# Performance work log

Hardware: AMD Instinct MI355X
Metric: run time of the kernel (lower is better)

## Reference

```python
import jax, jax.numpy as jnp
import numpy as np

B, D_IN, D_OUT, N_SUBNET, G = 16384, 512, 512, 8, 2


def setup_inputs() -> dict:
    key = jax.random.key(0)
    k_x, k_g, k_w = jax.random.split(key, 3)
    x = jax.random.normal(k_x, (B, D_IN), dtype=jnp.float32)
    groups = jax.random.randint(k_g, (B, G), 0, N_SUBNET, dtype=jnp.int32)
    # per-expert Dense params (the 'subnets')
    W = jax.random.normal(k_w, (N_SUBNET, D_IN, D_OUT), dtype=jnp.float32) * (1.0 / np.sqrt(D_IN))
    b = jnp.zeros((N_SUBNET, D_OUT), dtype=jnp.float32)
    return {"x": x, "groups": groups, "W": W, "b": b}


def reference(x, groups, W, b):
    """SubnetGate: one-hot gated dispatch to per-group subnets + combine.

    Faithful math: gates = one_hot(groups[:, group_col], n_subnet);
    out = sum_e gates[:, e] * subnet_e(x). Since gates are one-hot the
    combine selects exactly one expert output per row (gate weight 1.0).
    """
    group_col = 0
    n_subnet = W.shape[0]
    idx_group = groups[:, group_col]                     # [B]
    gates = jax.nn.one_hot(idx_group, n_subnet, dtype=x.dtype)  # [B, E]
    # run every expert on the full batch (dense reference for the
    # gather-compute-scatter kernel), then gate-combine
    expert_out = jnp.einsum("bi,eio->beo", x, W) + b[None, :, :]  # [B, E, O]
    out = jnp.einsum("be,beo->bo", gates, expert_out)             # [B, O]
    return out
```

## Files before the change

### kernel.cpp

```cpp
#include <hip/hip_runtime.h>
#include <hip/hip_bf16.h>


#define NROWS   16384
#define KDIM    512
#define NDIM    512
#define NEXP    8
#define BM      256
#define BN      128
#define NT_PER  4
#define KT_PER  8
#define MC_PER  9
#define TILE_ELEMS (BN * 64)
#define WS_ROWLIST_OFF 4096
#define WS_WT_OFF      (4096 + NEXP * NROWS * 4)
#define WS_XG_OFF      (WS_WT_OFF + (size_t)NEXP * NT_PER * KT_PER * TILE_ELEMS * 2)
#define WS_NEEDED      (WS_XG_OFF + (size_t)NROWS * KDIM * 2)

typedef __bf16        bf16x8 __attribute__((ext_vector_type(8)));
typedef float         f32x4  __attribute__((ext_vector_type(4)));
typedef unsigned int  u32x4  __attribute__((ext_vector_type(4)));

__device__ __forceinline__ unsigned int f2bf_u(float f) {
    unsigned int u = __builtin_bit_cast(unsigned int, f);
    return (u + 0x7FFFu + ((u >> 16) & 1u)) >> 16;
}

__device__ __forceinline__ void gl_lds16(const void* g, void* l) {
    __builtin_amdgcn_global_load_lds(
        (const __attribute__((address_space(1))) unsigned int*)g,
        (__attribute__((address_space(3))) unsigned int*)l, 16, 0, 0);
}

__device__ __forceinline__ bf16x8 pack_bf8(f32x4 lo, f32x4 hi) {
    u32x4 w;
    w.x = f2bf_u(lo.x) | (f2bf_u(lo.y) << 16);
    w.y = f2bf_u(lo.z) | (f2bf_u(lo.w) << 16);
    w.z = f2bf_u(hi.x) | (f2bf_u(hi.y) << 16);
    w.w = f2bf_u(hi.z) | (f2bf_u(hi.w) << 16);
    return __builtin_bit_cast(bf16x8, w);
}

__global__ void prep_kernel(const float* __restrict__ W,
                            const float* __restrict__ x,
                            const int* __restrict__ groups,
                            int* __restrict__ counts,
                            int* __restrict__ rowlist,
                            unsigned short* __restrict__ Wtile,
                            unsigned short* __restrict__ xg) {
    const int bid = blockIdx.x;
    const int tid = threadIdx.x;

    if (bid < 8) {
        __shared__ int wcnt_s[4];
        __shared__ int woff_s[4];
        __shared__ int runb;
        const int e  = bid;
        const int w  = tid >> 6;
        const int ln = tid & 63;
        const unsigned long long below = (ln == 63) ? ~0ull >> 1
                                                    : (1ull << ln) - 1;
        int* dst = rowlist + e * NROWS;
        if (tid == 0) runb = 0;
        __syncthreads();
        for (int it = 0; it < NROWS / 2048; ++it) {
            int rbase = it * 2048 + tid * 8;
            u32x4 g0 = *(const u32x4*)&groups[rbase * 2];
            u32x4 g1 = *(const u32x4*)&groups[rbase * 2 + 4];
            u32x4 g2 = *(const u32x4*)&groups[rbase * 2 + 8];
            u32x4 g3 = *(const u32x4*)&groups[rbase * 2 + 12];
            bool h[8] = {(int)g0.x == e, (int)g0.z == e,
                         (int)g1.x == e, (int)g1.z == e,
                         (int)g2.x == e, (int)g2.z == e,
                         (int)g3.x == e, (int)g3.z == e};
            unsigned long long m[8];
            int c[8], tot = 0;
            #pragma unroll
            for (int jj = 0; jj < 8; ++jj) {
                m[jj] = __ballot(h[jj]);
                c[jj] = __popcll(m[jj]);
                tot += c[jj];
            }
            if (ln == 0) wcnt_s[w] = tot;
            __syncthreads();
            if (tid == 0) {
                int s = runb;
                #pragma unroll
                for (int i = 0; i < 4; ++i) { woff_s[i] = s; s += wcnt_s[i]; }
                runb = s;
            }
            __syncthreads();
            int base = woff_s[w];
            #pragma unroll
            for (int jj = 0; jj < 8; ++jj) {
                if (h[jj]) dst[base + __popcll(m[jj] & below)] = rbase + jj;
                base += c[jj];
            }
            __syncthreads();
        }
        if (tid == 0) counts[e] = runb;
    } else if (bid < 1032) {
        __shared__ __align__(16) unsigned short tl4[32 * 64];
        const int tb   = bid - 8;
        const int tile = tb >> 2;
        const int qq   = tb & 3;
        const int e  = tile >> 5;
        const int nt = (tile >> 3) & 3;
        const int kt = tile & 7;
        const float* Wb = W + (size_t)e * (KDIM * NDIM);

        const int n   = qq * 32 + (tid & 31);
        const int g   = tid >> 5;
        const int col = nt * BN + n;
        unsigned int p[4];
        #pragma unroll
        for (int jj = 0; jj < 4; ++jj) {
            int k0 = kt * 64 + g * 8 + jj * 2;
            unsigned int lo = f2bf_u(Wb[(size_t)k0 * NDIM + col]);
            unsigned int hi = f2bf_u(Wb[(size_t)(k0 + 1) * NDIM + col]);
            p[jj] = lo | (hi << 16);
        }
        *(u32x4*)&tl4[(n & 31) * 64 + (g ^ (n & 7)) * 8] = *(const u32x4*)p;
        __syncthreads();
        unsigned short* dst = Wtile + (size_t)tile * TILE_ELEMS
                                    + ((size_t)qq * 256 + tid) * 8;
        *(u32x4*)dst = *(const u32x4*)&tl4[tid * 8];
    } else {
        const size_t base = ((size_t)(bid - 1032) * 256 + tid) * 16;
        f32x4 v0 = *(const f32x4*)&x[base];
        f32x4 v1 = *(const f32x4*)&x[base + 4];
        f32x4 v2 = *(const f32x4*)&x[base + 8];
        f32x4 v3 = *(const f32x4*)&x[base + 12];
        *(bf16x8*)&xg[base]     = pack_bf8(v0, v1);
        *(bf16x8*)&xg[base + 8] = pack_bf8(v2, v3);
    }
}


extern __shared__ __align__(16) unsigned short Bsm[];

#define LOAD_A_XG(QT, AR)                                                    \
    {                                                                        \
        _Pragma("unroll")                                                    \
        for (int _kh = 0; _kh < 4; ++_kh) {                                  \
            int _k0 = (QT) * 128 + _kh * 32 + q * 8;                         \
            AR[0][_kh] = *(const bf16x8*)(arow0 + _k0);                      \
            AR[1][_kh] = *(const bf16x8*)(arow1 + _k0);                      \
        }                                                                    \
    }

#define LOAD_A_F32(QT, AR)                                                   \
    {                                                                        \
        _Pragma("unroll")                                                    \
        for (int _kh = 0; _kh < 4; ++_kh) {                                  \
            int _k0 = (QT) * 128 + _kh * 32 + q * 8;                         \
            const float* _p0 = afrow0 + _k0;                                 \
            const float* _p1 = afrow1 + _k0;                                 \
            AR[0][_kh] = pack_bf8(*(const f32x4*)_p0, *(const f32x4*)(_p0 + 4)); \
            AR[1][_kh] = pack_bf8(*(const f32x4*)_p1, *(const f32x4*)(_p1 + 4)); \
        }                                                                    \
    }

#define COMPUTE_Q(QT, AR)                                                    \
    {                                                                        \
        _Pragma("unroll")                                                    \
        for (int _kh = 0; _kh < 4; ++_kh) {                                  \
            const int _t  = (QT) * 4 + _kh;                                  \
            const int _kt = _t >> 1;                                         \
            const int _g  = (_t & 1) * 4 + q;                                \
            _Pragma("unroll")                                                \
            for (int _ni = 0; _ni < 8; ++_ni) {                              \
                int _n = _ni * 16 + l15;                                     \
                bf16x8 _bf = *(const bf16x8*)&Bsm[_kt * TILE_ELEMS +         \
                             _n * 64 + (_g ^ (_n & 7)) * 8];                 \
                acc[0][_ni] = __builtin_amdgcn_mfma_f32_16x16x32_bf16(       \
                    AR[0][_kh], _bf, acc[0][_ni], 0, 0, 0);                  \
                acc[1][_ni] = __builtin_amdgcn_mfma_f32_16x16x32_bf16(       \
                    AR[1][_kh], _bf, acc[1][_ni], 0, 0, 0);                  \
            }                                                                \
        }                                                                    \
    }

#define KLOOP(LOADA)                                                         \
    {                                                                        \
        LOADA(1, aR)                                                         \
        COMPUTE_Q(0, aQ)                                                     \
        LOADA(2, aQ)                                                         \
        COMPUTE_Q(1, aR)                                                     \
        LOADA(3, aR)                                                         \
        COMPUTE_Q(2, aQ)                                                     \
        COMPUTE_Q(3, aR)                                                     \
    }

__global__ __launch_bounds__(512, 1)
void gemm_kernel(const float* __restrict__ x,
                 const unsigned short* __restrict__ xg,
                 const int* __restrict__ counts,
                 const int* __restrict__ rowlist,
                 const unsigned short* __restrict__ Wtile,
                 const float* __restrict__ bias,
                 float* __restrict__ out) {
    const int bid = blockIdx.x;
    const int e   = bid & 7;
    const int j   = bid >> 3;
    const int ns  = j & 3;
    const int mc  = j >> 2;
    const int cnt = counts[e];
    const int rb  = mc * BM;
    if (rb >= cnt) return;
    int m_valid = cnt - rb;
    if (m_valid > BM) m_valid = BM;
    const int* rl = rowlist + e * NROWS + rb;

    const int tid = threadIdx.x;
    const int w   = tid >> 6;
    const int ln  = tid & 63;
    const int q   = ln >> 4;
    const int l15 = ln & 15;
    const int wm  = w * 32;

    const unsigned short* wt =
        Wtile + (size_t)((e * NT_PER + ns) * KT_PER) * TILE_ELEMS;

    #pragma unroll
    for (int it = 0; it < 16; ++it) {
        int off = (it * 512 + tid) * 8;
        gl_lds16(wt + off, &Bsm[off]);
    }

    const int r0i = wm + l15;
    const int r1i = wm + 16 + l15;
    const int ri0 = (r0i < m_valid) ? r0i : 0;
    const int ri1 = (r1i < m_valid) ? r1i : 0;

    f32x4 acc[2][8];
    #pragma unroll
    for (int mi = 0; mi < 2; ++mi)
        #pragma unroll
        for (int ni = 0; ni < 8; ++ni)
            acc[mi][ni] = (f32x4){0.f, 0.f, 0.f, 0.f};

    bf16x8 aQ[2][4], aR[2][4];

    if (xg != nullptr) {
        const unsigned short* arow0 = xg + (size_t)rl[ri0] * KDIM;
        const unsigned short* arow1 = xg + (size_t)rl[ri1] * KDIM;
        LOAD_A_XG(0, aQ)
        asm volatile("s_waitcnt vmcnt(8)" ::: "memory");
        __builtin_amdgcn_s_barrier();
        KLOOP(LOAD_A_XG)
    } else {
        const float* afrow0 = x + (size_t)rl[ri0] * KDIM;
        const float* afrow1 = x + (size_t)rl[ri1] * KDIM;
        LOAD_A_F32(0, aQ)
        asm volatile("s_waitcnt vmcnt(16)" ::: "memory");
        __builtin_amdgcn_s_barrier();
        KLOOP(LOAD_A_F32)
    }

    int grow[2][4];
    #pragma unroll
    for (int mi = 0; mi < 2; ++mi)
        #pragma unroll
        for (int r = 0; r < 4; ++r) {
            int mloc = wm + mi * 16 + q * 4 + r;
            grow[mi][r] = (mloc < m_valid) ? rl[mloc] : -1;
        }
    const int ncol0 = ns * BN;
    #pragma unroll
    for (int ni = 0; ni < 8; ++ni) {
        int col = ncol0 + ni * 16 + l15;
        float bv = bias[e * NDIM + col];
        #pragma unroll
        for (int mi = 0; mi < 2; ++mi)
            #pragma unroll
            for (int r = 0; r < 4; ++r)
                if (grow[mi][r] >= 0)
                    out[(size_t)grow[mi][r] * NDIM + col] = acc[mi][ni][r] + bv;
    }
}

extern "C" void kernel_launch(void* const* d_in, const int* in_sizes, int n_in,
                              void* d_out, int out_size, void* d_ws, size_t ws_size,
                              hipStream_t stream) {
    const float* x      = (const float*)d_in[0];
    const int*   groups = (const int*)d_in[1];
    const float* W      = (const float*)d_in[2];
    const float* b      = (const float*)d_in[3];
    float*       out    = (float*)d_out;

    char* ws = (char*)d_ws;
    int*            counts  = (int*)ws;
    int*            rowlist = (int*)(ws + WS_ROWLIST_OFF);
    unsigned short* Wtile   = (unsigned short*)(ws + WS_WT_OFF);
    const bool use_xg = (ws_size >= WS_NEEDED);
    unsigned short* xg = use_xg ? (unsigned short*)(ws + WS_XG_OFF) : nullptr;

    static bool attr_set = false;
    if (!attr_set) {
        hipFuncSetAttribute((const void*)gemm_kernel,
                            hipFuncAttributeMaxDynamicSharedMemorySize,
                            KT_PER * TILE_ELEMS * 2);
        attr_set = true;
    }

    prep_kernel<<<use_xg ? 3080 : 1032, 256, 0, stream>>>(
        W, x, groups, counts, rowlist, Wtile, xg);
    gemm_kernel<<<NEXP * NT_PER * MC_PER, 512, KT_PER * TILE_ELEMS * 2, stream>>>(
        x, xg, counts, rowlist, Wtile, b, out);
}
```

Baseline: 131.1 us.

## Fuse W bf16 conversion into persistent GEMM blocks, drop x pre-conversion pass

The prep kernel now only builds the per-expert row lists. The W fp32-to-bf16 tiling moves into the GEMM kernel, where each block converts its W slice straight into LDS. The separate bf16 copy of x is removed and the GEMM always reads fp32 x and packs it in registers. The GEMM grid becomes 8 slots per expert/N-tile, each looping over M-chunks so the LDS W tile is reused across chunks. This saves the extra passes and workspace traffic for W and x, at the cost of strided uncoalesced W reads in every block, roughly double the bytes for A loads, and no overlap between the W load and the first A load.

```diff
diff --git a/kernel.cpp b/kernel.cpp
--- a/kernel.cpp
+++ b/kernel.cpp
@@ -10,12 +10,9 @@
 #define BN      128
 #define NT_PER  4
 #define KT_PER  8
-#define MC_PER  9
+#define SLOTS   8
 #define TILE_ELEMS (BN * 64)
 #define WS_ROWLIST_OFF 4096
-#define WS_WT_OFF      (4096 + NEXP * NROWS * 4)
-#define WS_XG_OFF      (WS_WT_OFF + (size_t)NEXP * NT_PER * KT_PER * TILE_ELEMS * 2)
-#define WS_NEEDED      (WS_XG_OFF + (size_t)NROWS * KDIM * 2)
 
 typedef __bf16        bf16x8 __attribute__((ext_vector_type(8)));
 typedef float         f32x4  __attribute__((ext_vector_type(4)));
@@ -24,12 +21,6 @@
 __device__ __forceinline__ unsigned int f2bf_u(float f) {
     unsigned int u = __builtin_bit_cast(unsigned int, f);
     return (u + 0x7FFFu + ((u >> 16) & 1u)) >> 16;
-}
-
-__device__ __forceinline__ void gl_lds16(const void* g, void* l) {
-    __builtin_amdgcn_global_load_lds(
-        (const __attribute__((address_space(1))) unsigned int*)g,
-        (__attribute__((address_space(3))) unsigned int*)l, 16, 0, 0);
 }
 
 __device__ __forceinline__ bf16x8 pack_bf8(f32x4 lo, f32x4 hi) {
@@ -41,113 +32,61 @@
     return __builtin_bit_cast(bf16x8, w);
 }
 
-__global__ void prep_kernel(const float* __restrict__ W,
-                            const float* __restrict__ x,
-                            const int* __restrict__ groups,
+__global__ void prep_kernel(const int* __restrict__ groups,
                             int* __restrict__ counts,
-                            int* __restrict__ rowlist,
-                            unsigned short* __restrict__ Wtile,
-                            unsigned short* __restrict__ xg) {
-    const int bid = blockIdx.x;
+                            int* __restrict__ rowlist) {
+    __shared__ int wcnt_s[4];
+    __shared__ int woff_s[4];
+    __shared__ int runb;
     const int tid = threadIdx.x;
-
-    if (bid < 8) {
-        __shared__ int wcnt_s[4];
-        __shared__ int woff_s[4];
-        __shared__ int runb;
-        const int e  = bid;
-        const int w  = tid >> 6;
-        const int ln = tid & 63;
-        const unsigned long long below = (ln == 63) ? ~0ull >> 1
-                                                    : (1ull << ln) - 1;
-        int* dst = rowlist + e * NROWS;
-        if (tid == 0) runb = 0;
+    const int e   = blockIdx.x;
+    const int w   = tid >> 6;
+    const int ln  = tid & 63;
+    const unsigned long long below = (ln == 63) ? ~0ull >> 1
+                                                : (1ull << ln) - 1;
+    int* dst = rowlist + e * NROWS;
+    if (tid == 0) runb = 0;
+    __syncthreads();
+    for (int it = 0; it < NROWS / 2048; ++it) {
+        int rbase = it * 2048 + tid * 8;
+        u32x4 g0 = *(const u32x4*)&groups[rbase * 2];
+        u32x4 g1 = *(const u32x4*)&groups[rbase * 2 + 4];
+        u32x4 g2 = *(const u32x4*)&groups[rbase * 2 + 8];
+        u32x4 g3 = *(const u32x4*)&groups[rbase * 2 + 12];
+        bool h[8] = {(int)g0.x == e, (int)g0.z == e,
+                     (int)g1.x == e, (int)g1.z == e,
+                     (int)g2.x == e, (int)g2.z == e,
+                     (int)g3.x == e, (int)g3.z == e};
+        unsigned long long m[8];
+        int c[8], tot = 0;
+        #pragma unroll
+        for (int jj = 0; jj < 8; ++jj) {
+            m[jj] = __ballot(h[jj]);
+            c[jj] = __popcll(m[jj]);
+            tot += c[jj];
+        }
+        if (ln == 0) wcnt_s[w] = tot;
         __syncthreads();
-        for (int it = 0; it < NROWS / 2048; ++it) {
-            int rbase = it * 2048 + tid * 8;
-            u32x4 g0 = *(const u32x4*)&groups[rbase * 2];
-            u32x4 g1 = *(const u32x4*)&groups[rbase * 2 + 4];
-            u32x4 g2 = *(const u32x4*)&groups[rbase * 2 + 8];
-            u32x4 g3 = *(const u32x4*)&groups[rbase * 2 + 12];
-            bool h[8] = {(int)g0.x == e, (int)g0.z == e,
-                         (int)g1.x == e, (int)g1.z == e,
-                         (int)g2.x == e, (int)g2.z == e,
-                         (int)g3.x == e, (int)g3.z == e};
-            unsigned long long m[8];
-            int c[8], tot = 0;
-            #pragma unroll
-            for (int jj = 0; jj < 8; ++jj) {
-                m[jj] = __ballot(h[jj]);
-                c[jj] = __popcll(m[jj]);
-                tot += c[jj];
-            }
-            if (ln == 0) wcnt_s[w] = tot;
-            __syncthreads();
-            if (tid == 0) {
-                int s = runb;
-                #pragma unroll
-                for (int i = 0; i < 4; ++i) { woff_s[i] = s; s += wcnt_s[i]; }
-                runb = s;
-            }
-            __syncthreads();
-            int base = woff_s[w];
-            #pragma unroll
-            for (int jj = 0; jj < 8; ++jj) {
-                if (h[jj]) dst[base + __popcll(m[jj] & below)] = rbase + jj;
-                base += c[jj];
-            }
-            __syncthreads();
-        }
-        if (tid == 0) counts[e] = runb;
-    } else if (bid < 1032) {
-        __shared__ __align__(16) unsigned short tl4[32 * 64];
-        const int tb   = bid - 8;
-        const int tile = tb >> 2;
-        const int qq   = tb & 3;
-        const int e  = tile >> 5;
-        const int nt = (tile >> 3) & 3;
-        const int kt = tile & 7;
-        const float* Wb = W + (size_t)e * (KDIM * NDIM);
-
-        const int n   = qq * 32 + (tid & 31);
-        const int g   = tid >> 5;
-        const int col = nt * BN + n;
-        unsigned int p[4];
-        #pragma unroll
-        for (int jj = 0; jj < 4; ++jj) {
-            int k0 = kt * 64 + g * 8 + jj * 2;
-            unsigned int lo = f2bf_u(Wb[(size_t)k0 * NDIM + col]);
-            unsigned int hi = f2bf_u(Wb[(size_t)(k0 + 1) * NDIM + col]);
-            p[jj] = lo | (hi << 16);
-        }
-        *(u32x4*)&tl4[(n & 31) * 64 + (g ^ (n & 7)) * 8] = *(const u32x4*)p;
+        if (tid == 0) {
+            int s = runb;
+            #pragma unroll
+            for (int i = 0; i < 4; ++i) { woff_s[i] = s; s += wcnt_s[i]; }
+            runb = s;
+        }
         __syncthreads();
-        unsigned short* dst = Wtile + (size_t)tile * TILE_ELEMS
-                                    + ((size_t)qq * 256 + tid) * 8;
-        *(u32x4*)dst = *(const u32x4*)&tl4[tid * 8];
-    } else {
-        const size_t base = ((size_t)(bid - 1032) * 256 + tid) * 16;
-        f32x4 v0 = *(const f32x4*)&x[base];
-        f32x4 v1 = *(const f32x4*)&x[base + 4];
-        f32x4 v2 = *(const f32x4*)&x[base + 8];
-        f32x4 v3 = *(const f32x4*)&x[base + 12];
-        *(bf16x8*)&xg[base]     = pack_bf8(v0, v1);
-        *(bf16x8*)&xg[base + 8] = pack_bf8(v2, v3);
-    }
+        int base = woff_s[w];
+        #pragma unroll
+        for (int jj = 0; jj < 8; ++jj) {
+            if (h[jj]) dst[base + __popcll(m[jj] & below)] = rbase + jj;
+            base += c[jj];
+        }
+        __syncthreads();
+    }
+    if (tid == 0) counts[e] = runb;
 }
 
 
 extern __shared__ __align__(16) unsigned short Bsm[];
-
-#define LOAD_A_XG(QT, AR)                                                    \
-    {                                                                        \
-        _Pragma("unroll")                                                    \
-        for (int _kh = 0; _kh < 4; ++_kh) {                                  \
-            int _k0 = (QT) * 128 + _kh * 32 + q * 8;                         \
-            AR[0][_kh] = *(const bf16x8*)(arow0 + _k0);                      \
-            AR[1][_kh] = *(const bf16x8*)(arow1 + _k0);                      \
-        }                                                                    \
-    }
 
 #define LOAD_A_F32(QT, AR)                                                   \
     {                                                                        \
@@ -181,36 +120,19 @@
         }                                                                    \
     }
 
-#define KLOOP(LOADA)                                                         \
-    {                                                                        \
-        LOADA(1, aR)                                                         \
-        COMPUTE_Q(0, aQ)                                                     \
-        LOADA(2, aQ)                                                         \
-        COMPUTE_Q(1, aR)                                                     \
-        LOADA(3, aR)                                                         \
-        COMPUTE_Q(2, aQ)                                                     \
-        COMPUTE_Q(3, aR)                                                     \
-    }
-
 __global__ __launch_bounds__(512, 1)
 void gemm_kernel(const float* __restrict__ x,
-                 const unsigned short* __restrict__ xg,
                  const int* __restrict__ counts,
                  const int* __restrict__ rowlist,
-                 const unsigned short* __restrict__ Wtile,
+                 const float* __restrict__ W,
                  const float* __restrict__ bias,
                  float* __restrict__ out) {
-    const int bid = blockIdx.x;
-    const int e   = bid & 7;
-    const int j   = bid >> 3;
-    const int ns  = j & 3;
-    const int mc  = j >> 2;
-    const int cnt = counts[e];
-    const int rb  = mc * BM;
-    if (rb >= cnt) return;
-    int m_valid = cnt - rb;
-    if (m_valid > BM) m_valid = BM;
-    const int* rl = rowlist + e * NROWS + rb;
+    const int bid  = blockIdx.x;
+    const int e    = bid & 7;
+    const int ns   = (bid >> 3) & 3;
+    const int slot = bid >> 5;
+    const int cnt  = counts[e];
+    if (slot * BM >= cnt) return;
 
     const int tid = threadIdx.x;
     const int w   = tid >> 6;
@@ -219,64 +141,79 @@
     const int l15 = ln & 15;
     const int wm  = w * 32;
 
-    const unsigned short* wt =
-        Wtile + (size_t)((e * NT_PER + ns) * KT_PER) * TILE_ELEMS;
-
+    const float* Wb = W + (size_t)e * (KDIM * NDIM) + ns * BN;
     #pragma unroll
     for (int it = 0; it < 16; ++it) {
-        int off = (it * 512 + tid) * 8;
-        gl_lds16(wt + off, &Bsm[off]);
-    }
-
-    const int r0i = wm + l15;
-    const int r1i = wm + 16 + l15;
-    const int ri0 = (r0i < m_valid) ? r0i : 0;
-    const int ri1 = (r1i < m_valid) ? r1i : 0;
-
-    f32x4 acc[2][8];
-    #pragma unroll
-    for (int mi = 0; mi < 2; ++mi)
-        #pragma unroll
-        for (int ni = 0; ni < 8; ++ni)
-            acc[mi][ni] = (f32x4){0.f, 0.f, 0.f, 0.f};
-
-    bf16x8 aQ[2][4], aR[2][4];
-
-    if (xg != nullptr) {
-        const unsigned short* arow0 = xg + (size_t)rl[ri0] * KDIM;
-        const unsigned short* arow1 = xg + (size_t)rl[ri1] * KDIM;
-        LOAD_A_XG(0, aQ)
-        asm volatile("s_waitcnt vmcnt(8)" ::: "memory");
-        __builtin_amdgcn_s_barrier();
-        KLOOP(LOAD_A_XG)
-    } else {
+        int gid = it * 512 + tid;
+        int kt  = gid >> 10;
+        int rem = gid & 1023;
+        int n   = rem & 127;
+        int g   = rem >> 7;
+        int k0  = kt * 64 + g * 8;
+        unsigned int p[4];
+        #pragma unroll
+        for (int jj = 0; jj < 4; ++jj) {
+            unsigned int lo = f2bf_u(Wb[(size_t)(k0 + jj * 2) * NDIM + n]);
+            unsigned int hi = f2bf_u(Wb[(size_t)(k0 + jj * 2 + 1) * NDIM + n]);
+            p[jj] = lo | (hi << 16);
+        }
+        *(u32x4*)&Bsm[kt * TILE_ELEMS + n * 64 + (g ^ (n & 7)) * 8] =
+            *(const u32x4*)p;
+    }
+    __syncthreads();
+
+    const int ncol0 = ns * BN;
+
+    for (int mc = slot; mc * BM < cnt; mc += SLOTS) {
+        const int rb = mc * BM;
+        int m_valid = cnt - rb;
+        if (m_valid > BM) m_valid = BM;
+        const int* rl = rowlist + e * NROWS + rb;
+
+        const int r0i = wm + l15;
+        const int r1i = wm + 16 + l15;
+        const int ri0 = (r0i < m_valid) ? r0i : 0;
+        const int ri1 = (r1i < m_valid) ? r1i : 0;
         const float* afrow0 = x + (size_t)rl[ri0] * KDIM;
         const float* afrow1 = x + (size_t)rl[ri1] * KDIM;
+
+        f32x4 acc[2][8];
+        #pragma unroll
+        for (int mi = 0; mi < 2; ++mi)
+            #pragma unroll
+            for (int ni = 0; ni < 8; ++ni)
+                acc[mi][ni] = (f32x4){0.f, 0.f, 0.f, 0.f};
+
+        bf16x8 aQ[2][4], aR[2][4];
         LOAD_A_F32(0, aQ)
-        asm volatile("s_waitcnt vmcnt(16)" ::: "memory");
-        __builtin_amdgcn_s_barrier();
-        KLOOP(LOAD_A_F32)
-    }
-
-    int grow[2][4];
-    #pragma unroll
-    for (int mi = 0; mi < 2; ++mi)
-        #pragma unroll
-        for (int r = 0; r < 4; ++r) {
-            int mloc = wm + mi * 16 + q * 4 + r;
-            grow[mi][r] = (mloc < m_valid) ? rl[mloc] : -1;
-        }
-    const int ncol0 = ns * BN;
-    #pragma unroll
-    for (int ni = 0; ni < 8; ++ni) {
-        int col = ncol0 + ni * 16 + l15;
-        float bv = bias[e * NDIM + col];
+        LOAD_A_F32(1, aR)
+        COMPUTE_Q(0, aQ)
+        LOAD_A_F32(2, aQ)
+        COMPUTE_Q(1, aR)
+        LOAD_A_F32(3, aR)
+        COMPUTE_Q(2, aQ)
+        COMPUTE_Q(3, aR)
+
+        int grow[2][4];
         #pragma unroll
         for (int mi = 0; mi < 2; ++mi)
             #pragma unroll
-            for (int r = 0; r < 4; ++r)
-                if (grow[mi][r] >= 0)
-                    out[(size_t)grow[mi][r] * NDIM + col] = acc[mi][ni][r] + bv;
+            for (int r = 0; r < 4; ++r) {
+                int mloc = wm + mi * 16 + q * 4 + r;
+                grow[mi][r] = (mloc < m_valid) ? rl[mloc] : -1;
+            }
+        #pragma unroll
+        for (int ni = 0; ni < 8; ++ni) {
+            int col = ncol0 + ni * 16 + l15;
+            float bv = bias[e * NDIM + col];
+            #pragma unroll
+            for (int mi = 0; mi < 2; ++mi)
+                #pragma unroll
+                for (int r = 0; r < 4; ++r)
+                    if (grow[mi][r] >= 0)
+                        out[(size_t)grow[mi][r] * NDIM + col] =
+                            acc[mi][ni][r] + bv;
+        }
     }
 }
 
@@ -290,11 +227,8 @@
     float*       out    = (float*)d_out;
 
     char* ws = (char*)d_ws;
-    int*            counts  = (int*)ws;
-    int*            rowlist = (int*)(ws + WS_ROWLIST_OFF);
-    unsigned short* Wtile   = (unsigned short*)(ws + WS_WT_OFF);
-    const bool use_xg = (ws_size >= WS_NEEDED);
-    unsigned short* xg = use_xg ? (unsigned short*)(ws + WS_XG_OFF) : nullptr;
+    int*  counts  = (int*)ws;
+    int*  rowlist = (int*)(ws + WS_ROWLIST_OFF);
 
     static bool attr_set = false;
     if (!attr_set) {
@@ -304,8 +238,7 @@
         attr_set = true;
     }
 
-    prep_kernel<<<use_xg ? 3080 : 1032, 256, 0, stream>>>(
-        W, x, groups, counts, rowlist, Wtile, xg);
-    gemm_kernel<<<NEXP * NT_PER * MC_PER, 512, KT_PER * TILE_ELEMS * 2, stream>>>(
-        x, xg, counts, rowlist, Wtile, b, out);
-}
+    prep_kernel<<<NEXP, 256, 0, stream>>>(groups, counts, rowlist);
+    gemm_kernel<<<NEXP * NT_PER * SLOTS, 512, KT_PER * TILE_ELEMS * 2, stream>>>(
+        x, counts, rowlist, W, b, out);
+}
```

Result: slower. 295.8 us (+125.6%).
